# Optimization experiments

Measured on AMD Instinct MI355X. Metric: run time of the kernel, lower is better.

Reference implementation:

```python
import jax, jax.numpy as jnp
import numpy as np

NEG = -1e6  # matches torch masked value of -1000000.0
EPS = 1e-5


def setup_inputs() -> dict:
    key = jax.random.key(0)
    k1, k2, k3, k4, k5, k6 = jax.random.split(key, 6)
    B, H, L, D = 2, 16, 2048, 128
    BH = B * H
    return {
        "queries": jax.random.normal(k1, (BH, L, D), dtype=jnp.float32),
        "keys": jax.random.normal(k2, (BH, L, D), dtype=jnp.float32),
        "values": jax.random.normal(k3, (BH, L, D), dtype=jnp.float32),
        "q_mult": jax.random.normal(k4, (B, L, D), dtype=jnp.float32),
        "kv_mult": jax.random.normal(k5, (B, L, D), dtype=jnp.float32),
        "valid_lens": jax.random.randint(k6, (BH,), 0, L, dtype=jnp.int64),
        "num_heads": 16,
    }


def reference(queries, keys, values, q_mult, kv_mult, valid_lens, num_heads):
    # queries/keys/values: [BH, L, d]; q_mult/kv_mult: [B, L, d_m]; valid_lens: [BH]
    d = queries.shape[-1]
    Lk = keys.shape[1]
    scale = 1.0 / jnp.sqrt(jnp.asarray(d, dtype=queries.dtype))
    scores = jnp.einsum('bqd,bkd->bqk', queries, keys) * scale  # [BH, Lq, Lk]

    # custom additive multiplicative-interaction term, Frobenius-normalized per batch element
    mult_ = jnp.einsum('bqd,bkd->bqk', q_mult, kv_mult)  # [B, Lq, Lk]
    fro = jnp.sqrt(jnp.sum(mult_ * mult_, axis=(1, 2), keepdims=True))
    mult_ = mult_ / (fro + EPS)
    mult_ = jnp.repeat(mult_, num_heads, axis=0)  # [BH, Lq, Lk]

    # masked softmax over keys: valid_lens is per-(batch*head), broadcast over queries
    key_mask = jnp.arange(Lk)[None, None, :] < valid_lens[:, None, None]  # [BH, 1, Lk]
    scores = jnp.where(key_mask, scores, NEG)
    attn = jax.nn.softmax(scores, axis=-1) + mult_  # after_softmax=True path

    # dropout is identity (p=0 / eval)
    return jnp.einsum('bqk,bkd->bqd', attn, values)
```

## Files before the change

kernel.cpp:

```cpp
#include <hip/hip_runtime.h>


typedef __attribute__((ext_vector_type(8))) __bf16 bf16x8;
typedef __attribute__((ext_vector_type(16))) float f32x16;
typedef __attribute__((ext_vector_type(4))) unsigned int u32x4;

#define DEV static __device__ __forceinline__

constexpr int LL = 2048, DD = 128, BH = 32;
constexpr float SCALE = 0.08838834764831845f;
constexpr float NEGV = -1e6f;

DEV unsigned pkb(float a, float b) {
  union { __bf16 h[2]; unsigned u; } x;
  x.h[0] = (__bf16)a; x.h[1] = (__bf16)b;
  return x.u;
}
DEV f32x16 mfma32(bf16x8 a, bf16x8 b, f32x16 c) {
  return __builtin_amdgcn_mfma_f32_32x32x16_bf16(a, b, c, 0, 0, 0);
}
DEV void gl16(const void* g, void* l) {
  __builtin_amdgcn_global_load_lds(
      (const __attribute__((address_space(1))) unsigned int*)g,
      (__attribute__((address_space(3))) unsigned int*)l, 16, 0, 0);
}

__global__ __launch_bounds__(256)
void mega_pre(const float* __restrict__ K, const float* __restrict__ V,
              const float* __restrict__ qm, const float* __restrict__ km,
              char* __restrict__ Kb, char* __restrict__ Vt,
              float* __restrict__ Gq, float* __restrict__ Gk,
              float* __restrict__ Mp) {
  __shared__ __align__(16) char smem[16384];
  const int bx = blockIdx.x, tid = threadIdx.x;

  if (bx < 512) {
    float (*skv)[64] = (float(*)[64])smem;
    float (*sv)[128] = (float(*)[128])(smem + 4096);
    int bh = bx & 31, b = bh >> 4, kc = (bx >> 5) & 7, z = (bx >> 8) & 1;
    int l0 = kc * 256;
    int j0 = (tid & 31) * 4, i0 = (tid >> 5) * 8;
    float acc[8][4];
#pragma unroll
    for (int i = 0; i < 8; ++i)
#pragma unroll
      for (int qq = 0; qq < 4; ++qq) acc[i][qq] = 0.f;
    for (int c = 0; c < 16; ++c) {
      __syncthreads();
      {
        int rr = tid >> 4, c4 = (tid & 15) * 4;
        *(float4*)&skv[rr][c4] =
            *(const float4*)(km + (size_t)(b * LL + l0 + c * 16 + rr) * DD + z * 64 + c4);
#pragma unroll
        for (int x = 0; x < 2; ++x) {
          int id2 = x * 256 + tid;
          int r2 = id2 >> 5, c42 = (id2 & 31) * 4;
          *(float4*)&sv[r2][c42] =
              *(const float4*)(V + (size_t)(bh * LL + l0 + c * 16 + r2) * DD + c42);
        }
      }
      __syncthreads();
#pragma unroll
      for (int ll = 0; ll < 16; ++ll) {
        float4 a = *(const float4*)&sv[ll][j0];
        float4 k0 = *(const float4*)&skv[ll][i0];
        float4 k1 = *(const float4*)&skv[ll][i0 + 4];
        float kk[8] = {k0.x, k0.y, k0.z, k0.w, k1.x, k1.y, k1.z, k1.w};
#pragma unroll
        for (int ii = 0; ii < 8; ++ii) {
          acc[ii][0] += kk[ii] * a.x;
          acc[ii][1] += kk[ii] * a.y;
          acc[ii][2] += kk[ii] * a.z;
          acc[ii][3] += kk[ii] * a.w;
        }
      }
    }
    float* dst = Mp + (((size_t)bh * 8 + kc) << 14) + (size_t)(z * 64 + i0) * 128 + j0;
#pragma unroll
    for (int ii = 0; ii < 8; ++ii)
      *(float4*)(dst + (size_t)ii * 128) = *(float4*)&acc[ii][0];

  } else if (bx < 640) {
    float (*s)[128] = (float(*)[128])smem;
    int g = bx - 512;
    int ib = g & 7, lc = (g >> 3) & 3, wb = g >> 5;
    int which = wb >> 1, b = wb & 1;
    const float* A = (which ? km : qm) + (size_t)b * LL * DD;
    float* G = (which ? Gk : Gq) + (size_t)b * DD * DD;
    int i0 = ib * 16 + (tid >> 7) * 8, j = tid & 127;
    int l0 = lc * 512;
    float acc[8];
#pragma unroll
    for (int i = 0; i < 8; ++i) acc[i] = 0.f;
    for (int ch = 0; ch < 16; ++ch) {
      __syncthreads();
#pragma unroll
      for (int i = 0; i < 4; ++i) {
        int c = i * 256 + tid;
        int row = c >> 5, c4 = (c & 31) * 4;
        *(float4*)&s[row][c4] =
            *(const float4*)(A + (size_t)(l0 + ch * 32 + row) * DD + c4);
      }
      __syncthreads();
#pragma unroll
      for (int ll = 0; ll < 32; ++ll) {
        float aj = s[ll][j];
#pragma unroll
        for (int ii = 0; ii < 8; ++ii) acc[ii] += s[ll][i0 + ii] * aj;
      }
    }
#pragma unroll
    for (int ii = 0; ii < 8; ++ii)
      atomicAdd(&G[(size_t)(i0 + ii) * DD + j], acc[ii]);

  } else if (bx < 1664) {
    int pk = bx - 640;
#pragma unroll
    for (int i = 0; i < 4; ++i) {
      int cid = i * 262144 + pk * 256 + tid;
      int h = cid >> 15, k = (cid >> 4) & 2047, c = cid & 15;
      const float* p = K + ((size_t)h * LL + k) * DD + c * 8;
      float4 x0 = *(const float4*)p, x1 = *(const float4*)(p + 4);
      u32x4 v;
      v.x = pkb(x0.x, x0.y); v.y = pkb(x0.z, x0.w);
      v.z = pkb(x1.x, x1.y); v.w = pkb(x1.z, x1.w);
      char* dst = Kb + (((size_t)h * 64 + (k >> 5)) << 13) + ((k & 31) << 8) +
                  ((c ^ (k & 15)) << 4);
      *(u32x4*)dst = v;
    }

  } else {
    float (*sV)[128] = (float(*)[128])smem;
    int pv = bx - 1664;
    int h = pv >> 6, kt = pv & 63;
    const float* src = V + ((size_t)h * LL + kt * 32) * DD;
#pragma unroll
    for (int i = 0; i < 4; ++i) {
      int c = i * 256 + tid;
      int row = c >> 5, c4 = (c & 31) * 4;
      *(float4*)&sV[row][c4] = *(const float4*)(src + (size_t)row * DD + c4);
    }
    __syncthreads();
    char* dstb = Vt + (((size_t)h * 64 + kt) << 13);
#pragma unroll
    for (int i = 0; i < 2; ++i) {
      int c = i * 256 + tid;
      int d = c >> 2, kk8 = c & 3;
      u32x4 v;
      v.x = pkb(sV[kk8 * 8 + 0][d], sV[kk8 * 8 + 1][d]);
      v.y = pkb(sV[kk8 * 8 + 2][d], sV[kk8 * 8 + 3][d]);
      v.z = pkb(sV[kk8 * 8 + 4][d], sV[kk8 * 8 + 5][d]);
      v.w = pkb(sV[kk8 * 8 + 6][d], sV[kk8 * 8 + 7][d]);
      *(u32x4*)(dstb + d * 64 + ((kk8 ^ ((d >> 1) & 3)) << 4)) = v;
    }
  }
}

__global__ __launch_bounds__(256)
void k_post(const float* __restrict__ Gq, const float* __restrict__ Gk,
            float* __restrict__ fro, const float* __restrict__ Mp,
            char* __restrict__ MT) {
  int bx = blockIdx.x, tid = threadIdx.x;
  if (bx < 2) {
    int b = bx;
    const float* gq = Gq + (size_t)b * DD * DD;
    const float* gk = Gk + (size_t)b * DD * DD;
    float acc = 0.f;
    for (int i = tid; i < DD * DD; i += 256) acc += gq[i] * gk[i];
#pragma unroll
    for (int m = 32; m; m >>= 1) acc += __shfl_xor(acc, m);
    __shared__ float sbuf[4];
    if ((tid & 63) == 0) sbuf[tid >> 6] = acc;
    __syncthreads();
    if (tid == 0) fro[b] = sqrtf(sbuf[0] + sbuf[1] + sbuf[2] + sbuf[3]);
  } else {
    int g = bx - 2;
    int bh = g >> 2, kq = (g & 3) * 32;
    int k = kq + (tid >> 3), d0 = (tid & 7) * 16;
    float acc[16];
#pragma unroll
    for (int i = 0; i < 16; ++i) acc[i] = 0.f;
#pragma unroll
    for (int s = 0; s < 8; ++s) {
      const float* p = Mp + (((size_t)bh * 8 + s) << 14) + (size_t)k * 128 + d0;
#pragma unroll
      for (int i = 0; i < 4; ++i) {
        float4 v = *(const float4*)(p + i * 4);
        acc[4 * i + 0] += v.x; acc[4 * i + 1] += v.y;
        acc[4 * i + 2] += v.z; acc[4 * i + 3] += v.w;
      }
    }
    char* dst = MT + (size_t)bh * 32768;
#pragma unroll
    for (int j = 0; j < 16; ++j) {
      int d = d0 + j;
      union { __bf16 h; unsigned short u; } cv;
      cv.h = (__bf16)acc[j];
      *(unsigned short*)(dst + d * 256 + (((k >> 3) ^ (d & 15)) << 4) + (k & 7) * 2) = cv.u;
    }
  }
}

template <int MODE>
__global__ __launch_bounds__(128, 2)
void k_flash(const char* __restrict__ KbG, const char* __restrict__ VtG,
             const char* __restrict__ MT, const float* __restrict__ fro,
             const float* __restrict__ Qf, const float* __restrict__ Kf,
             const float* __restrict__ Vf, const float* __restrict__ qmf,
             const int* __restrict__ vl, float* __restrict__ out) {
  __shared__ __align__(16) char lds[MODE ? 16384 : 32768];

  const int qt = blockIdx.x, bh = blockIdx.y, b = bh >> 4;
  const int tid = threadIdx.x, w = tid >> 6, lane = tid & 63;
  const int r32 = lane & 31, hi = lane >> 5;
  const int vlen = vl[bh];
  const size_t base = (size_t)bh * LL * DD;
  const int q = qt * 64 + w * 32 + r32;

  bf16x8 qfr[8];
#pragma unroll
  for (int ks = 0; ks < 8; ++ks) {
    const float* p = Qf + base + (size_t)q * DD + ks * 16 + hi * 8;
    float4 x0 = *(const float4*)p, x1 = *(const float4*)(p + 4);
    union { unsigned u[4]; bf16x8 v; } u;
    u.u[0] = pkb(x0.x * SCALE, x0.y * SCALE);
    u.u[1] = pkb(x0.z * SCALE, x0.w * SCALE);
    u.u[2] = pkb(x1.x * SCALE, x1.y * SCALE);
    u.u[3] = pkb(x1.z * SCALE, x1.w * SCALE);
    qfr[ks] = u.v;
  }

  f32x16 o[4];
#pragma unroll
  for (int dt = 0; dt < 4; ++dt)
#pragma unroll
    for (int e = 0; e < 16; ++e) o[dt][e] = 0.f;
  float mrun = -3e38f, lrun = 0.f;

  int nt = (vlen == 0) ? 64 : ((vlen + 31) >> 5);

  auto compute = [&](const char* Kl, const char* Vl, int kbase) {
    f32x16 s0;
#pragma unroll
    for (int e = 0; e < 16; ++e) s0[e] = 0.f;
    __builtin_amdgcn_s_setprio(1);
#pragma unroll
    for (int ks = 0; ks < 8; ++ks) {
      bf16x8 a0 = *(const bf16x8*)(Kl + r32 * 256 + (((2 * ks + hi) ^ (r32 & 15)) << 4));
      s0 = mfma32(a0, qfr[ks], s0);
    }
    __builtin_amdgcn_s_setprio(0);

    if (kbase + 32 > vlen) {
#pragma unroll
      for (int e = 0; e < 16; ++e) {
        int k0 = kbase + (e & 3) + 8 * (e >> 2) + 4 * hi;
        if (k0 >= vlen) s0[e] = NEGV;
      }
    }
    f32x16 mx = s0;
#pragma unroll
    for (int st = 8; st; st >>= 1)
#pragma unroll
      for (int e = 0; e < st; ++e) mx[e] = fmaxf(mx[e], mx[e + st]);
    float pm = fmaxf(mx[0], __shfl_xor(mx[0], 32));

    if (!__all(pm <= mrun + 8.f)) {
      float mn = fmaxf(mrun, pm);
      float al = __expf(mrun - mn);
      lrun *= al;
#pragma unroll
      for (int dt = 0; dt < 4; ++dt)
#pragma unroll
        for (int e = 0; e < 16; ++e) o[dt][e] *= al;
      mrun = mn;
    }
#pragma unroll
    for (int e = 0; e < 16; ++e) s0[e] = __expf(s0[e] - mrun);
    f32x16 sm = s0;
#pragma unroll
    for (int st = 8; st; st >>= 1)
#pragma unroll
      for (int e = 0; e < st; ++e) sm[e] += sm[e + st];
    lrun += sm[0];

    bf16x8 PA[2];
#pragma unroll
    for (int ks = 0; ks < 2; ++ks) {
      int bb = ks * 8;
      unsigned x1 = pkb(s0[bb + 0], s0[bb + 1]);
      unsigned x2 = pkb(s0[bb + 2], s0[bb + 3]);
      unsigned y1 = pkb(s0[bb + 4], s0[bb + 5]);
      unsigned y2 = pkb(s0[bb + 6], s0[bb + 7]);
      unsigned sx1 = __shfl_xor(x1, 32), sx2 = __shfl_xor(x2, 32);
      unsigned sy1 = __shfl_xor(y1, 32), sy2 = __shfl_xor(y2, 32);
      union { unsigned u[4]; bf16x8 v; } pu;
      pu.u[0] = hi ? sy1 : x1;
      pu.u[1] = hi ? sy2 : x2;
      pu.u[2] = hi ? y1 : sx1;
      pu.u[3] = hi ? y2 : sx2;
      PA[ks] = pu.v;
    }
    __builtin_amdgcn_s_setprio(1);
#pragma unroll
    for (int dt = 0; dt < 4; ++dt)
#pragma unroll
      for (int ks = 0; ks < 2; ++ks) {
        bf16x8 av = *(const bf16x8*)(Vl + (dt * 32 + r32) * 64 +
                                     (((2 * ks + hi) ^ ((r32 >> 1) & 3)) << 4));
        o[dt] = mfma32(av, PA[ks], o[dt]);
      }
    __builtin_amdgcn_s_setprio(0);
  };

  if (MODE == 0) {
    auto stage = [&](int t, int c2) {
      const char* gk = KbG + (((size_t)bh * 64 + t) << 13) + tid * 16;
      const char* gv = VtG + (((size_t)bh * 64 + t) << 13) + tid * 16;
      char* lk = lds + c2 * 16384 + tid * 16;
      char* lv = lds + c2 * 16384 + 8192 + tid * 16;
#pragma unroll
      for (int i = 0; i < 4; ++i) {
        gl16(gk + i * 2048, lk + i * 2048);
        gl16(gv + i * 2048, lv + i * 2048);
      }
    };
    stage(0, 0);
    int cur = 0;
    for (int t = 0; t < nt; ++t) {
      if (t + 1 < nt) {
        stage(t + 1, cur ^ 1);
        asm volatile("s_waitcnt vmcnt(8)" ::: "memory");
      } else {
        asm volatile("s_waitcnt vmcnt(0)" ::: "memory");
      }
      __builtin_amdgcn_sched_barrier(0);
      __builtin_amdgcn_s_barrier();
      __builtin_amdgcn_sched_barrier(0);
      compute(lds + cur * 16384, lds + cur * 16384 + 8192, t * 32);
      __builtin_amdgcn_sched_barrier(0);
      __builtin_amdgcn_s_barrier();
      __builtin_amdgcn_sched_barrier(0);
      cur ^= 1;
    }
  } else {
    char* Kl = lds;
    char* Vl = lds + 8192;
    for (int t = 0; t < nt; ++t) {
      int kbase = t * 32;
      __syncthreads();
#pragma unroll
      for (int i = 0; i < 4; ++i) {
        int c = i * 128 + tid;
        int kk = c >> 4, sl = c & 15;
        const float* p = Kf + base + (size_t)(kbase + kk) * DD + sl * 8;
        float4 x0 = *(const float4*)p, x1 = *(const float4*)(p + 4);
        u32x4 v;
        v.x = pkb(x0.x, x0.y); v.y = pkb(x0.z, x0.w);
        v.z = pkb(x1.x, x1.y); v.w = pkb(x1.z, x1.w);
        *(u32x4*)(Kl + (kk << 8) + ((sl ^ (kk & 15)) << 4)) = v;
      }
#pragma unroll
      for (int i = 0; i < 4; ++i) {
        int c = i * 128 + tid;
        int d = c >> 2, kk8 = c & 3;
        float t0[8];
#pragma unroll
        for (int j = 0; j < 8; ++j)
          t0[j] = Vf[base + (size_t)(kbase + kk8 * 8 + j) * DD + d];
        u32x4 v;
        v.x = pkb(t0[0], t0[1]); v.y = pkb(t0[2], t0[3]);
        v.z = pkb(t0[4], t0[5]); v.w = pkb(t0[6], t0[7]);
        *(u32x4*)(Vl + d * 64 + ((kk8 ^ ((d >> 1) & 3)) << 4)) = v;
      }
      __syncthreads();
      compute(Kl, Vl, kbase);
    }
  }

  float lt = lrun + __shfl_xor(lrun, 32);
  float inv = 1.f / lt;
#pragma unroll
  for (int dt = 0; dt < 4; ++dt)
#pragma unroll
    for (int e = 0; e < 16; ++e) o[dt][e] *= inv;

  if (MODE == 0) {
    float invf = 1.f / (fro[b] + 1e-5f);
    bf16x8 qb[8];
#pragma unroll
    for (int ks = 0; ks < 8; ++ks) {
      const float* p = qmf + ((size_t)b * LL + q) * DD + ks * 16 + hi * 8;
      float4 x0 = *(const float4*)p, x1 = *(const float4*)(p + 4);
      union { unsigned u[4]; bf16x8 v; } u;
      u.u[0] = pkb(x0.x * invf, x0.y * invf);
      u.u[1] = pkb(x0.z * invf, x0.w * invf);
      u.u[2] = pkb(x1.x * invf, x1.y * invf);
      u.u[3] = pkb(x1.z * invf, x1.w * invf);
      qb[ks] = u.v;
    }
    const char* MTb = MT + (size_t)bh * 32768;
#pragma unroll
    for (int kc = 0; kc < 8; ++kc)
#pragma unroll
      for (int dt = 0; dt < 4; ++dt) {
        bf16x8 av = *(const bf16x8*)(MTb + (dt * 32 + r32) * 256 +
                                     (((2 * kc + hi) ^ (r32 & 15)) << 4));
        o[dt] = mfma32(av, qb[kc], o[dt]);
      }
  }

  float* op = out + base + (size_t)q * DD;
#pragma unroll
  for (int dt = 0; dt < 4; ++dt)
#pragma unroll
    for (int rq = 0; rq < 4; ++rq) {
      float4 v;
      v.x = o[dt][4 * rq + 0];
      v.y = o[dt][4 * rq + 1];
      v.z = o[dt][4 * rq + 2];
      v.w = o[dt][4 * rq + 3];
      *(float4*)(op + dt * 32 + rq * 8 + hi * 4) = v;
    }
}

__global__ void k_gram(const float* __restrict__ qm, const float* __restrict__ km,
                       float* __restrict__ Gq, float* __restrict__ Gk) {
  int which = blockIdx.z >> 1, b = blockIdx.z & 1;
  const float* A = (which ? km : qm) + (size_t)b * LL * DD;
  float* G = (which ? Gk : Gq) + (size_t)b * DD * DD;
  int i0 = blockIdx.x * 8;
  int l0 = blockIdx.y * 512;
  __shared__ float s[32][128];
  float acc[8];
#pragma unroll
  for (int i = 0; i < 8; ++i) acc[i] = 0.f;
  for (int ch = 0; ch < 16; ++ch) {
    __syncthreads();
    for (int rr = 0; rr < 32; ++rr)
      s[rr][threadIdx.x] = A[(size_t)(l0 + ch * 32 + rr) * DD + threadIdx.x];
    __syncthreads();
    for (int ll = 0; ll < 32; ++ll) {
      float aj = s[ll][threadIdx.x];
#pragma unroll
      for (int ii = 0; ii < 8; ++ii) acc[ii] += s[ll][i0 + ii] * aj;
    }
  }
#pragma unroll
  for (int ii = 0; ii < 8; ++ii)
    atomicAdd(&G[(size_t)(i0 + ii) * DD + threadIdx.x], acc[ii]);
}

__global__ void k_fro(const float* __restrict__ Gq, const float* __restrict__ Gk,
                      float* __restrict__ fro) {
  int b = blockIdx.x;
  const float* gq = Gq + (size_t)b * DD * DD;
  const float* gk = Gk + (size_t)b * DD * DD;
  float acc = 0.f;
  for (int i = threadIdx.x; i < DD * DD; i += 256) acc += gq[i] * gk[i];
#pragma unroll
  for (int m = 32; m; m >>= 1) acc += __shfl_xor(acc, m);
  __shared__ float sbuf[4];
  if ((threadIdx.x & 63) == 0) sbuf[threadIdx.x >> 6] = acc;
  __syncthreads();
  if (threadIdx.x == 0) fro[b] = sqrtf(sbuf[0] + sbuf[1] + sbuf[2] + sbuf[3]);
}

__global__ void k_M_atomic(const float* __restrict__ km, const float* __restrict__ Vf,
                           float* __restrict__ M) {
  int bh = blockIdx.x, b = bh >> 4;
  int l0 = blockIdx.y * 128;
  __shared__ float skv[16][128];
  __shared__ float sv[16][128];
  int j0 = (threadIdx.x & 31) * 4;
  int i0 = (threadIdx.x >> 5) * 16;
  float acc[16][4];
#pragma unroll
  for (int i = 0; i < 16; ++i)
#pragma unroll
    for (int qq = 0; qq < 4; ++qq) acc[i][qq] = 0.f;
  for (int c = 0; c < 8; ++c) {
    __syncthreads();
    for (int x = 0; x < 8; ++x) {
      int idx = x * 256 + threadIdx.x;
      int rr = idx >> 7, cc = idx & 127;
      skv[rr][cc] = km[(size_t)(b * LL + l0 + c * 16 + rr) * DD + cc];
      sv[rr][cc] = Vf[(size_t)(bh * LL + l0 + c * 16 + rr) * DD + cc];
    }
    __syncthreads();
    for (int ll = 0; ll < 16; ++ll) {
      float a0 = sv[ll][j0], a1 = sv[ll][j0 + 1];
      float a2 = sv[ll][j0 + 2], a3 = sv[ll][j0 + 3];
#pragma unroll
      for (int ii = 0; ii < 16; ++ii) {
        float kv = skv[ll][i0 + ii];
        acc[ii][0] += kv * a0;
        acc[ii][1] += kv * a1;
        acc[ii][2] += kv * a2;
        acc[ii][3] += kv * a3;
      }
    }
  }
#pragma unroll
  for (int ii = 0; ii < 16; ++ii)
#pragma unroll
    for (int qq = 0; qq < 4; ++qq)
      atomicAdd(&M[(size_t)bh * DD * DD + (size_t)(i0 + ii) * DD + j0 + qq],
                acc[ii][qq]);
}

__global__ void k_multadd(const float* __restrict__ qm, const float* __restrict__ M,
                          const float* __restrict__ fro, float* __restrict__ out) {
  int bh = blockIdx.y, b = bh >> 4;
  int l = blockIdx.x * 128 + (threadIdx.x & 127);
  int dh = (threadIdx.x >> 7) * 64;
  float inv = 1.0f / (fro[b] + 1e-5f);
  const float* qrow = qm + ((size_t)b * LL + l) * DD;
  const float* Mb = M + (size_t)bh * DD * DD + dh;
  float acc[64];
#pragma unroll
  for (int i = 0; i < 64; ++i) acc[i] = 0.f;
  for (int k = 0; k < 128; ++k) {
    float qv = qrow[k];
    const float4* m4 = (const float4*)(Mb + (size_t)k * DD);
#pragma unroll
    for (int i = 0; i < 16; ++i) {
      float4 mm = m4[i];
      acc[4 * i + 0] += qv * mm.x;
      acc[4 * i + 1] += qv * mm.y;
      acc[4 * i + 2] += qv * mm.z;
      acc[4 * i + 3] += qv * mm.w;
    }
  }
  float* op = out + ((size_t)bh * LL + l) * DD + dh;
#pragma unroll
  for (int i = 0; i < 16; ++i) {
    float4 ov = ((float4*)op)[i];
    ov.x += acc[4 * i + 0] * inv;
    ov.y += acc[4 * i + 1] * inv;
    ov.z += acc[4 * i + 2] * inv;
    ov.w += acc[4 * i + 3] * inv;
    ((float4*)op)[i] = ov;
  }
}

extern "C" void kernel_launch(void* const* d_in, const int* in_sizes, int n_in,
                              void* d_out, int out_size, void* d_ws, size_t ws_size,
                              hipStream_t stream) {
  (void)in_sizes; (void)n_in; (void)out_size;
  const float* Q = (const float*)d_in[0];
  const float* K = (const float*)d_in[1];
  const float* V = (const float*)d_in[2];
  const float* qm = (const float*)d_in[3];
  const float* km = (const float*)d_in[4];
  const int* vl = (const int*)d_in[5];
  float* out = (float*)d_out;

  char* ws = (char*)d_ws;
  const size_t off_Gq = 0;
  const size_t off_Gk = 131072;
  const size_t off_fro = 262144;
  const size_t off_MT = 294912;
  const size_t off_Kb = off_MT + 1048576;
  const size_t szb = (size_t)BH * LL * DD * 2;
  const size_t off_Vt = off_Kb + szb;
  const size_t off_end = off_Vt + szb;
  bool fits = ws_size >= off_end;

  float* Gq = (float*)(ws + off_Gq);
  float* Gk = (float*)(ws + off_Gk);
  float* fro = (float*)(ws + off_fro);
  char* MT = ws + off_MT;

  if (fits) {
    float* Mp = (float*)d_out;
    hipMemsetAsync(ws, 0, off_fro + 256, stream);
    mega_pre<<<3712, 256, 0, stream>>>(K, V, qm, km, ws + off_Kb, ws + off_Vt,
                                       Gq, Gk, Mp);
    k_post<<<130, 256, 0, stream>>>(Gq, Gk, fro, Mp, MT);
    k_flash<0><<<dim3(32, 32), 128, 0, stream>>>(ws + off_Kb, ws + off_Vt, MT, fro,
                                                 Q, K, V, qm, vl, out);
  } else {
    float* Mw = (float*)(ws + off_MT);
    hipMemsetAsync(ws, 0, off_MT + 2097152, stream);
    k_gram<<<dim3(16, 4, 4), 128, 0, stream>>>(qm, km, Gq, Gk);
    k_fro<<<2, 256, 0, stream>>>(Gq, Gk, fro);
    k_flash<1><<<dim3(32, 32), 128, 0, stream>>>(nullptr, nullptr, nullptr, nullptr,
                                                 Q, K, V, qm, vl, out);
    k_M_atomic<<<dim3(32, 16), 256, 0, stream>>>(km, V, Mw);
    k_multadd<<<dim3(16, 32), 256, 0, stream>>>(qm, Mw, fro, out);
  }
}
```

Baseline: 173.3 us.

## Use single-wave flash blocks with V loaded straight into registers

The main flash kernel now runs one wavefront per block over 32 queries, on a grid twice as large. K tiles are still double-buffered in LDS through async global-to-LDS loads. V fragments are now loaded straight from global memory into double-buffered registers, so no block barriers are needed. The intent is to remove s_barrier sync and V's LDS traffic and to raise the number of independent waves. The costs are higher register pressure and every wave re-reading the K/V tiles with no sharing between two waves. The fallback path is split into its own kernel with unchanged logic.

```diff
diff --git a/kernel.cpp b/kernel.cpp
--- a/kernel.cpp
+++ b/kernel.cpp
@@ -201,21 +201,19 @@
   }
 }
 
-template <int MODE>
-__global__ __launch_bounds__(128, 2)
-void k_flash(const char* __restrict__ KbG, const char* __restrict__ VtG,
-             const char* __restrict__ MT, const float* __restrict__ fro,
-             const float* __restrict__ Qf, const float* __restrict__ Kf,
-             const float* __restrict__ Vf, const float* __restrict__ qmf,
-             const int* __restrict__ vl, float* __restrict__ out) {
-  __shared__ __align__(16) char lds[MODE ? 16384 : 32768];
+__global__ __launch_bounds__(64, 2)
+void k_flash1(const char* __restrict__ KbG, const char* __restrict__ VtG,
+              const char* __restrict__ MT, const float* __restrict__ fro,
+              const float* __restrict__ Qf, const float* __restrict__ qmf,
+              const int* __restrict__ vl, float* __restrict__ out) {
+  __shared__ __align__(16) char lds[16384];
 
   const int qt = blockIdx.x, bh = blockIdx.y, b = bh >> 4;
-  const int tid = threadIdx.x, w = tid >> 6, lane = tid & 63;
+  const int lane = threadIdx.x;
   const int r32 = lane & 31, hi = lane >> 5;
   const int vlen = vl[bh];
   const size_t base = (size_t)bh * LL * DD;
-  const int q = qt * 64 + w * 32 + r32;
+  const int q = qt * 32 + r32;
 
   bf16x8 qfr[8];
 #pragma unroll
@@ -239,7 +237,26 @@
 
   int nt = (vlen == 0) ? 64 : ((vlen + 31) >> 5);
 
-  auto compute = [&](const char* Kl, const char* Vl, int kbase) {
+  const char* kb = KbG + (((size_t)bh * 64) << 13);
+  const char* vb = VtG + (((size_t)bh * 64) << 13);
+
+  auto stageK = [&](int t, int c2) {
+    const char* gk = kb + ((size_t)t << 13) + lane * 16;
+    char* lk = lds + c2 * 8192 + lane * 16;
+#pragma unroll
+    for (int i = 0; i < 8; ++i) gl16(gk + i * 1024, lk + i * 1024);
+  };
+  auto loadV = [&](int t, u32x4* vr) {
+    const char* gv = vb + ((size_t)t << 13);
+#pragma unroll
+    for (int dt = 0; dt < 4; ++dt)
+#pragma unroll
+      for (int ks = 0; ks < 2; ++ks)
+        vr[dt * 2 + ks] = *(const u32x4*)(gv + (dt * 32 + r32) * 64 +
+                                          (((2 * ks + hi) ^ ((r32 >> 1) & 3)) << 4));
+  };
+
+  auto compute = [&](const char* Kl, const u32x4* vr, int kbase) {
     f32x16 s0;
 #pragma unroll
     for (int e = 0; e < 16; ++e) s0[e] = 0.f;
@@ -306,76 +323,37 @@
     for (int dt = 0; dt < 4; ++dt)
 #pragma unroll
       for (int ks = 0; ks < 2; ++ks) {
-        bf16x8 av = *(const bf16x8*)(Vl + (dt * 32 + r32) * 64 +
-                                     (((2 * ks + hi) ^ ((r32 >> 1) & 3)) << 4));
-        o[dt] = mfma32(av, PA[ks], o[dt]);
+        union { u32x4 w; bf16x8 v; } cv;
+        cv.w = vr[dt * 2 + ks];
+        o[dt] = mfma32(cv.v, PA[ks], o[dt]);
       }
     __builtin_amdgcn_s_setprio(0);
   };
 
-  if (MODE == 0) {
-    auto stage = [&](int t, int c2) {
-      const char* gk = KbG + (((size_t)bh * 64 + t) << 13) + tid * 16;
-      const char* gv = VtG + (((size_t)bh * 64 + t) << 13) + tid * 16;
-      char* lk = lds + c2 * 16384 + tid * 16;
-      char* lv = lds + c2 * 16384 + 8192 + tid * 16;
-#pragma unroll
-      for (int i = 0; i < 4; ++i) {
-        gl16(gk + i * 2048, lk + i * 2048);
-        gl16(gv + i * 2048, lv + i * 2048);
-      }
-    };
-    stage(0, 0);
-    int cur = 0;
-    for (int t = 0; t < nt; ++t) {
-      if (t + 1 < nt) {
-        stage(t + 1, cur ^ 1);
-        asm volatile("s_waitcnt vmcnt(8)" ::: "memory");
-      } else {
-        asm volatile("s_waitcnt vmcnt(0)" ::: "memory");
-      }
-      __builtin_amdgcn_sched_barrier(0);
-      __builtin_amdgcn_s_barrier();
-      __builtin_amdgcn_sched_barrier(0);
-      compute(lds + cur * 16384, lds + cur * 16384 + 8192, t * 32);
-      __builtin_amdgcn_sched_barrier(0);
-      __builtin_amdgcn_s_barrier();
-      __builtin_amdgcn_sched_barrier(0);
-      cur ^= 1;
-    }
-  } else {
-    char* Kl = lds;
-    char* Vl = lds + 8192;
-    for (int t = 0; t < nt; ++t) {
-      int kbase = t * 32;
-      __syncthreads();
-#pragma unroll
-      for (int i = 0; i < 4; ++i) {
-        int c = i * 128 + tid;
-        int kk = c >> 4, sl = c & 15;
-        const float* p = Kf + base + (size_t)(kbase + kk) * DD + sl * 8;
-        float4 x0 = *(const float4*)p, x1 = *(const float4*)(p + 4);
-        u32x4 v;
-        v.x = pkb(x0.x, x0.y); v.y = pkb(x0.z, x0.w);
-        v.z = pkb(x1.x, x1.y); v.w = pkb(x1.z, x1.w);
-        *(u32x4*)(Kl + (kk << 8) + ((sl ^ (kk & 15)) << 4)) = v;
-      }
-#pragma unroll
-      for (int i = 0; i < 4; ++i) {
-        int c = i * 128 + tid;
-        int d = c >> 2, kk8 = c & 3;
-        float t0[8];
-#pragma unroll
-        for (int j = 0; j < 8; ++j)
-          t0[j] = Vf[base + (size_t)(kbase + kk8 * 8 + j) * DD + d];
-        u32x4 v;
-        v.x = pkb(t0[0], t0[1]); v.y = pkb(t0[2], t0[3]);
-        v.z = pkb(t0[4], t0[5]); v.w = pkb(t0[6], t0[7]);
-        *(u32x4*)(Vl + d * 64 + ((kk8 ^ ((d >> 1) & 3)) << 4)) = v;
-      }
-      __syncthreads();
-      compute(Kl, Vl, kbase);
-    }
+  u32x4 vA[8], vB[8];
+  stageK(0, 0);
+  loadV(0, vA);
+  int t = 0;
+  while (true) {
+    if (t + 1 < nt) {
+      stageK(t + 1, 1); loadV(t + 1, vB);
+      asm volatile("s_waitcnt vmcnt(16)" ::: "memory");
+    } else {
+      asm volatile("s_waitcnt vmcnt(0)" ::: "memory");
+    }
+    __builtin_amdgcn_sched_barrier(0);
+    compute(lds, vA, t * 32);
+    if (++t >= nt) break;
+
+    if (t + 1 < nt) {
+      stageK(t + 1, 0); loadV(t + 1, vA);
+      asm volatile("s_waitcnt vmcnt(16)" ::: "memory");
+    } else {
+      asm volatile("s_waitcnt vmcnt(0)" ::: "memory");
+    }
+    __builtin_amdgcn_sched_barrier(0);
+    compute(lds + 8192, vB, t * 32);
+    if (++t >= nt) break;
   }
 
   float lt = lrun + __shfl_xor(lrun, 32);
@@ -385,7 +363,7 @@
 #pragma unroll
     for (int e = 0; e < 16; ++e) o[dt][e] *= inv;
 
-  if (MODE == 0) {
+  {
     float invf = 1.f / (fro[b] + 1e-5f);
     bf16x8 qb[8];
 #pragma unroll
@@ -420,6 +398,154 @@
       v.y = o[dt][4 * rq + 1];
       v.z = o[dt][4 * rq + 2];
       v.w = o[dt][4 * rq + 3];
+      *(float4*)(op + dt * 32 + rq * 8 + hi * 4) = v;
+    }
+}
+
+__global__ __launch_bounds__(128, 2)
+void k_flashF(const float* __restrict__ Qf, const float* __restrict__ Kf,
+              const float* __restrict__ Vf, const int* __restrict__ vl,
+              float* __restrict__ out) {
+  __shared__ __align__(16) char lds[16384];
+  const int qt = blockIdx.x, bh = blockIdx.y;
+  const int tid = threadIdx.x, w = tid >> 6, lane = tid & 63;
+  const int r32 = lane & 31, hi = lane >> 5;
+  const int vlen = vl[bh];
+  const size_t base = (size_t)bh * LL * DD;
+  const int q = qt * 64 + w * 32 + r32;
+
+  bf16x8 qfr[8];
+#pragma unroll
+  for (int ks = 0; ks < 8; ++ks) {
+    const float* p = Qf + base + (size_t)q * DD + ks * 16 + hi * 8;
+    float4 x0 = *(const float4*)p, x1 = *(const float4*)(p + 4);
+    union { unsigned u[4]; bf16x8 v; } u;
+    u.u[0] = pkb(x0.x * SCALE, x0.y * SCALE);
+    u.u[1] = pkb(x0.z * SCALE, x0.w * SCALE);
+    u.u[2] = pkb(x1.x * SCALE, x1.y * SCALE);
+    u.u[3] = pkb(x1.z * SCALE, x1.w * SCALE);
+    qfr[ks] = u.v;
+  }
+
+  f32x16 o[4];
+#pragma unroll
+  for (int dt = 0; dt < 4; ++dt)
+#pragma unroll
+    for (int e = 0; e < 16; ++e) o[dt][e] = 0.f;
+  float mrun = -3e38f, lrun = 0.f;
+  int nt = (vlen == 0) ? 64 : ((vlen + 31) >> 5);
+
+  char* Kl = lds;
+  char* Vl = lds + 8192;
+  for (int t = 0; t < nt; ++t) {
+    int kbase = t * 32;
+    __syncthreads();
+#pragma unroll
+    for (int i = 0; i < 4; ++i) {
+      int c = i * 128 + tid;
+      int kk = c >> 4, sl = c & 15;
+      const float* p = Kf + base + (size_t)(kbase + kk) * DD + sl * 8;
+      float4 x0 = *(const float4*)p, x1 = *(const float4*)(p + 4);
+      u32x4 v;
+      v.x = pkb(x0.x, x0.y); v.y = pkb(x0.z, x0.w);
+      v.z = pkb(x1.x, x1.y); v.w = pkb(x1.z, x1.w);
+      *(u32x4*)(Kl + (kk << 8) + ((sl ^ (kk & 15)) << 4)) = v;
+    }
+#pragma unroll
+    for (int i = 0; i < 4; ++i) {
+      int c = i * 128 + tid;
+      int d = c >> 2, kk8 = c & 3;
+      float t0[8];
+#pragma unroll
+      for (int j = 0; j < 8; ++j)
+        t0[j] = Vf[base + (size_t)(kbase + kk8 * 8 + j) * DD + d];
+      u32x4 v;
+      v.x = pkb(t0[0], t0[1]); v.y = pkb(t0[2], t0[3]);
+      v.z = pkb(t0[4], t0[5]); v.w = pkb(t0[6], t0[7]);
+      *(u32x4*)(Vl + d * 64 + ((kk8 ^ ((d >> 1) & 3)) << 4)) = v;
+    }
+    __syncthreads();
+
+    f32x16 s0;
+#pragma unroll
+    for (int e = 0; e < 16; ++e) s0[e] = 0.f;
+#pragma unroll
+    for (int ks = 0; ks < 8; ++ks) {
+      bf16x8 a0 = *(const bf16x8*)(Kl + r32 * 256 + (((2 * ks + hi) ^ (r32 & 15)) << 4));
+      s0 = mfma32(a0, qfr[ks], s0);
+    }
+    if (kbase + 32 > vlen) {
+#pragma unroll
+      for (int e = 0; e < 16; ++e) {
+        int k0 = kbase + (e & 3) + 8 * (e >> 2) + 4 * hi;
+        if (k0 >= vlen) s0[e] = NEGV;
+      }
+    }
+    f32x16 mx = s0;
+#pragma unroll
+    for (int st = 8; st; st >>= 1)
+#pragma unroll
+      for (int e = 0; e < st; ++e) mx[e] = fmaxf(mx[e], mx[e + st]);
+    float pm = fmaxf(mx[0], __shfl_xor(mx[0], 32));
+    if (!__all(pm <= mrun + 8.f)) {
+      float mn = fmaxf(mrun, pm);
+      float al = __expf(mrun - mn);
+      lrun *= al;
+#pragma unroll
+      for (int dt = 0; dt < 4; ++dt)
+#pragma unroll
+        for (int e = 0; e < 16; ++e) o[dt][e] *= al;
+      mrun = mn;
+    }
+#pragma unroll
+    for (int e = 0; e < 16; ++e) s0[e] = __expf(s0[e] - mrun);
+    f32x16 sm = s0;
+#pragma unroll
+    for (int st = 8; st; st >>= 1)
+#pragma unroll
+      for (int e = 0; e < st; ++e) sm[e] += sm[e + st];
+    lrun += sm[0];
+
+    bf16x8 PA[2];
+#pragma unroll
+    for (int ks = 0; ks < 2; ++ks) {
+      int bb = ks * 8;
+      unsigned x1 = pkb(s0[bb + 0], s0[bb + 1]);
+      unsigned x2 = pkb(s0[bb + 2], s0[bb + 3]);
+      unsigned y1 = pkb(s0[bb + 4], s0[bb + 5]);
+      unsigned y2 = pkb(s0[bb + 6], s0[bb + 7]);
+      unsigned sx1 = __shfl_xor(x1, 32), sx2 = __shfl_xor(x2, 32);
+      unsigned sy1 = __shfl_xor(y1, 32), sy2 = __shfl_xor(y2, 32);
+      union { unsigned u[4]; bf16x8 v; } pu;
+      pu.u[0] = hi ? sy1 : x1;
+      pu.u[1] = hi ? sy2 : x2;
+      pu.u[2] = hi ? y1 : sx1;
+      pu.u[3] = hi ? y2 : sx2;
+      PA[ks] = pu.v;
+    }
+#pragma unroll
+    for (int dt = 0; dt < 4; ++dt)
+#pragma unroll
+      for (int ks = 0; ks < 2; ++ks) {
+        bf16x8 av = *(const bf16x8*)(Vl + (dt * 32 + r32) * 64 +
+                                     (((2 * ks + hi) ^ ((r32 >> 1) & 3)) << 4));
+        o[dt] = mfma32(av, PA[ks], o[dt]);
+      }
+    __syncthreads();
+  }
+
+  float lt = lrun + __shfl_xor(lrun, 32);
+  float inv = 1.f / lt;
+  float* op = out + base + (size_t)q * DD;
+#pragma unroll
+  for (int dt = 0; dt < 4; ++dt)
+#pragma unroll
+    for (int rq = 0; rq < 4; ++rq) {
+      float4 v;
+      v.x = o[dt][4 * rq + 0] * inv;
+      v.y = o[dt][4 * rq + 1] * inv;
+      v.z = o[dt][4 * rq + 2] * inv;
+      v.w = o[dt][4 * rq + 3] * inv;
       *(float4*)(op + dt * 32 + rq * 8 + hi * 4) = v;
     }
 }
@@ -578,15 +704,14 @@
     mega_pre<<<3712, 256, 0, stream>>>(K, V, qm, km, ws + off_Kb, ws + off_Vt,
                                        Gq, Gk, Mp);
     k_post<<<130, 256, 0, stream>>>(Gq, Gk, fro, Mp, MT);
-    k_flash<0><<<dim3(32, 32), 128, 0, stream>>>(ws + off_Kb, ws + off_Vt, MT, fro,
-                                                 Q, K, V, qm, vl, out);
+    k_flash1<<<dim3(64, 32), 64, 0, stream>>>(ws + off_Kb, ws + off_Vt, MT, fro,
+                                              Q, qm, vl, out);
   } else {
     float* Mw = (float*)(ws + off_MT);
     hipMemsetAsync(ws, 0, off_MT + 2097152, stream);
     k_gram<<<dim3(16, 4, 4), 128, 0, stream>>>(qm, km, Gq, Gk);
     k_fro<<<2, 256, 0, stream>>>(Gq, Gk, fro);
-    k_flash<1><<<dim3(32, 32), 128, 0, stream>>>(nullptr, nullptr, nullptr, nullptr,
-                                                 Q, K, V, qm, vl, out);
+    k_flashF<<<dim3(32, 32), 128, 0, stream>>>(Q, K, V, vl, out);
     k_M_atomic<<<dim3(32, 16), 256, 0, stream>>>(km, V, Mw);
     k_multadd<<<dim3(16, 32), 256, 0, stream>>>(qm, Mw, fro, out);
   }
```

After: 170.3 us. Within noise of the previous version (-1.7%).
